# Optimization experiments

Hardware: AMD Instinct MI355X
Metric: run time of the kernel (lower is better)

Reference implementation:

```python
import jax, jax.numpy as jnp
import numpy as np

N = 4096      # (num_domains+1) * batch_size
F_IN = 512    # nfeat
HID = 64      # nhid per head
H = 8         # nheads
ALPHA = 0.2   # leaky-relu negative slope
EDGE_P = 0.01 # adjacency density


def setup_inputs() -> dict:
    key = jax.random.key(0)
    k1, k2, k3, k4 = jax.random.split(key, 4)
    x = jax.random.normal(k1, (N, F_IN), dtype=jnp.float32)
    adj = (jax.random.uniform(k2, (N, N)) < EDGE_P).astype(jnp.float32)
    # ensure self-loops so every row has at least one valid edge for softmax
    adj = jnp.maximum(adj, jnp.eye(N, dtype=jnp.float32))
    W = jax.random.normal(k3, (H, F_IN, HID), dtype=jnp.float32) * 0.1
    a = jax.random.normal(k4, (H, 2 * HID), dtype=jnp.float32) * 0.1
    return {"x": x, "adj": adj, "W": W, "a": a}


def reference(x, adj, W, a):
    # Wh: [H, N, HID] -- per-head linear projection
    Wh = jnp.einsum('nf,hfd->hnd', x, W)
    # additive attention logits: e_ij = leakyrelu(a1.Wh_i + a2.Wh_j)
    e_src = jnp.einsum('hnd,hd->hn', Wh, a[:, :HID])   # [H, N]
    e_dst = jnp.einsum('hnd,hd->hn', Wh, a[:, HID:])   # [H, N]
    e = jax.nn.leaky_relu(e_src[:, :, None] + e_dst[:, None, :], ALPHA)  # [H, N, N]
    e = jnp.where(adj[None] > 0, e, jnp.float32(-9e15))
    att = jax.nn.softmax(e, axis=-1)                    # masked softmax over neighbors
    h = jnp.einsum('hnm,hmd->hnd', att, Wh)             # [H, N, HID]
    h = jax.nn.elu(h)                                   # concat=True -> elu per head
    # concat heads: [N, H*HID]
    return jnp.transpose(h, (1, 0, 2)).reshape(N, H * HID)
```

## Files before the change

kernel.cpp:

```cpp
#include <hip/hip_runtime.h>
#include <hip/hip_bf16.h>
#include <math.h>

#define N_NODES 4096
#define F_IN    512
#define HID     64
#define H       8
#define NJ      512
#define ALPHA   0.2f

typedef __bf16 bf16x8 __attribute__((ext_vector_type(8)));
typedef float  f32x4  __attribute__((ext_vector_type(4)));

#define A_UNITS (N_NODES * F_IN / 4)
#define B_UNITS (NJ * F_IN)

__device__ __forceinline__ void split_bf16(float v, __bf16& hi, __bf16& lo) {
    hi = (__bf16)v;
    lo = (__bf16)(v - (float)hi);
}

__global__ __launch_bounds__(256) void conv_prep(const float* __restrict__ x,
                                                 const float* __restrict__ W,
                                                 __bf16* __restrict__ Ah,
                                                 __bf16* __restrict__ Al,
                                                 __bf16* __restrict__ Bth,
                                                 __bf16* __restrict__ Btl) {
    int id = blockIdx.x * 256 + threadIdx.x;
    if (id < A_UNITS) {
        float4 v = ((const float4*)x)[id];
        __bf16 h0, h1, h2, h3, l0, l1, l2, l3;
        split_bf16(v.x, h0, l0); split_bf16(v.y, h1, l1);
        split_bf16(v.z, h2, l2); split_bf16(v.w, h3, l3);
        __bf16* ph = Ah + (size_t)id * 4;
        __bf16* pl = Al + (size_t)id * 4;
        ph[0] = h0; ph[1] = h1; ph[2] = h2; ph[3] = h3;
        pl[0] = l0; pl[1] = l1; pl[2] = l2; pl[3] = l3;
    } else {
        int bid = id - A_UNITS;
        if (bid < B_UNITS) {
            int k = bid & (F_IN - 1);
            int j = bid >> 9;
            float v = W[(size_t)(j >> 6) * F_IN * HID + (size_t)k * HID + (j & 63)];
            __bf16 h, l;
            split_bf16(v, h, l);
            Bth[(size_t)j * F_IN + k] = h;
            Btl[(size_t)j * F_IN + k] = l;
        }
    }
}

__global__ __launch_bounds__(256) void wh_gemm_mfma(const __bf16* __restrict__ Ah,
                                                    const __bf16* __restrict__ Al,
                                                    const __bf16* __restrict__ Bth,
                                                    const __bf16* __restrict__ Btl,
                                                    float* __restrict__ Whf,
                                                    __bf16* __restrict__ Whb) {
    const int bm = blockIdx.x;
    const int bn = blockIdx.y;
    const int tid  = threadIdx.x;
    const int wave = tid >> 6;
    const int lane = tid & 63;
    const int lm = lane & 15;
    const int lq = lane >> 4;

    __shared__ __align__(16) __bf16 As_h[128][40];
    __shared__ __align__(16) __bf16 As_l[128][40];
    __shared__ __align__(16) __bf16 Bs_h[64][40];
    __shared__ __align__(16) __bf16 Bs_l[64][40];

    f32x4 acc[2][4];
    #pragma unroll
    for (int r = 0; r < 2; r++)
        #pragma unroll
        for (int c = 0; c < 4; c++)
            acc[r][c] = (f32x4){0.f, 0.f, 0.f, 0.f};

    for (int k0 = 0; k0 < F_IN; k0 += 32) {
        #pragma unroll
        for (int s = 0; s < 2; s++) {
            int idx = tid + s * 256;
            int m  = idx >> 2;
            int kk = (idx & 3) << 3;
            size_t g = (size_t)(bm * 128 + m) * F_IN + k0 + kk;
            *(uint4*)&As_h[m][kk] = *(const uint4*)(Ah + g);
            *(uint4*)&As_l[m][kk] = *(const uint4*)(Al + g);
        }
        {
            int n  = tid >> 2;
            int kk = (tid & 3) << 3;
            size_t g = (size_t)(bn * 64 + n) * F_IN + k0 + kk;
            *(uint4*)&Bs_h[n][kk] = *(const uint4*)(Bth + g);
            *(uint4*)&Bs_l[n][kk] = *(const uint4*)(Btl + g);
        }
        __syncthreads();

        bf16x8 afh[2], afl[2], bfh[4], bfl[4];
        #pragma unroll
        for (int r = 0; r < 2; r++) {
            int row = wave * 32 + r * 16 + lm;
            afh[r] = *(const bf16x8*)&As_h[row][lq * 8];
            afl[r] = *(const bf16x8*)&As_l[row][lq * 8];
        }
        #pragma unroll
        for (int c = 0; c < 4; c++) {
            int nrow = c * 16 + lm;
            bfh[c] = *(const bf16x8*)&Bs_h[nrow][lq * 8];
            bfl[c] = *(const bf16x8*)&Bs_l[nrow][lq * 8];
        }
        #pragma unroll
        for (int r = 0; r < 2; r++)
            #pragma unroll
            for (int c = 0; c < 4; c++) {
                acc[r][c] = __builtin_amdgcn_mfma_f32_16x16x32_bf16(afh[r], bfh[c], acc[r][c], 0, 0, 0);
                acc[r][c] = __builtin_amdgcn_mfma_f32_16x16x32_bf16(afh[r], bfl[c], acc[r][c], 0, 0, 0);
                acc[r][c] = __builtin_amdgcn_mfma_f32_16x16x32_bf16(afl[r], bfh[c], acc[r][c], 0, 0, 0);
            }
        __syncthreads();
    }

    #pragma unroll
    for (int r = 0; r < 2; r++)
        #pragma unroll
        for (int c = 0; c < 4; c++)
            #pragma unroll
            for (int reg = 0; reg < 4; reg++) {
                int row = bm * 128 + wave * 32 + r * 16 + lq * 4 + reg;
                int col = bn * 64 + c * 16 + lm;
                float v = acc[r][c][reg];
                Whf[(size_t)row * NJ + col] = v;
                Whb[(size_t)row * NJ + col] = (__bf16)v;
            }
}

__global__ __launch_bounds__(256) void src_dst(const float* __restrict__ Whf,
                                               const float* __restrict__ a,
                                               float* __restrict__ esrc,
                                               float* __restrict__ edst) {
    int gw   = blockIdx.x * 4 + (threadIdx.x >> 6);
    int lane = threadIdx.x & 63;
    int n = gw >> 3;
    int h = gw & 7;
    float v  = Whf[(size_t)n * NJ + h * HID + lane];
    float p1 = v * a[h * 2 * HID + lane];
    float p2 = v * a[h * 2 * HID + HID + lane];
    #pragma unroll
    for (int o = 32; o; o >>= 1) {
        p1 += __shfl_xor(p1, o);
        p2 += __shfl_xor(p2, o);
    }
    if (lane == 0) {
        esrc[h * N_NODES + n] = p1;
        edst[h * N_NODES + n] = p2;
    }
}

#define MAXN 192

__global__ __launch_bounds__(512) void gat_attn(const float* __restrict__ adj,
                                                const __bf16* __restrict__ Whb,
                                                const float* __restrict__ esrc,
                                                const float* __restrict__ edst,
                                                float* __restrict__ out) {
    const int i   = blockIdx.x;
    const int tid = threadIdx.x;
    __shared__ int   nbr[MAXN];
    __shared__ float att[H][MAXN];
    __shared__ float denom[H];
    __shared__ __align__(8) float2 part[256];
    __shared__ int   cnt;

    if (tid == 0) cnt = 0;
    __syncthreads();

    const float4* arow = (const float4*)(adj + (size_t)i * N_NODES);
    for (int v = tid; v < N_NODES / 4; v += 512) {
        float4 q = arow[v];
        if (q.x > 0.f) { int p = atomicAdd(&cnt, 1); if (p < MAXN) nbr[p] = v * 4 + 0; }
        if (q.y > 0.f) { int p = atomicAdd(&cnt, 1); if (p < MAXN) nbr[p] = v * 4 + 1; }
        if (q.z > 0.f) { int p = atomicAdd(&cnt, 1); if (p < MAXN) nbr[p] = v * 4 + 2; }
        if (q.w > 0.f) { int p = atomicAdd(&cnt, 1); if (p < MAXN) nbr[p] = v * 4 + 3; }
    }
    __syncthreads();
    int n = cnt;
    if (n > MAXN) n = MAXN;

    {
        const int lane = tid & 63;
        const int h    = tid >> 6;
        float es = esrc[h * N_NODES + i];
        float m = -1e30f;
        for (int j = lane; j < n; j += 64) {
            float lg = es + edst[h * N_NODES + nbr[j]];
            lg = lg > 0.f ? lg : ALPHA * lg;
            att[h][j] = lg;
            m = fmaxf(m, lg);
        }
        #pragma unroll
        for (int o = 32; o; o >>= 1) m = fmaxf(m, __shfl_xor(m, o));
        float s = 0.f;
        for (int j = lane; j < n; j += 64) {
            float w = __expf(att[h][j] - m);
            att[h][j] = w;
            s += w;
        }
        #pragma unroll
        for (int o = 32; o; o >>= 1) s += __shfl_xor(s, o);
        if (lane == 0) denom[h] = s;
    }
    __syncthreads();

    const int half = tid >> 8;
    const int t    = tid & 255;
    const int h    = t >> 5;
    const int dp   = t & 31;
    const __bf16* wb = Whb + h * HID + dp * 2;

    float acc0 = 0.f, acc1 = 0.f;
    #pragma unroll 4
    for (int j = half; j < n; j += 2) {
        int nb = nbr[j];
        float w = att[h][j];
        unsigned u = *(const unsigned*)(wb + (size_t)nb * NJ);
        float f0 = __uint_as_float(u << 16);
        float f1 = __uint_as_float(u & 0xffff0000u);
        acc0 += w * f0;
        acc1 += w * f1;
    }
    if (half == 1) part[t] = make_float2(acc0, acc1);
    __syncthreads();
    if (half == 0) {
        float2 p = part[t];
        float inv = 1.f / denom[h];
        float v0 = (acc0 + p.x) * inv;
        float v1 = (acc1 + p.y) * inv;
        v0 = v0 > 0.f ? v0 : expm1f(v0);
        v1 = v1 > 0.f ? v1 : expm1f(v1);
        *(float2*)(out + (size_t)i * NJ + h * HID + dp * 2) = make_float2(v0, v1);
    }
}

extern "C" void kernel_launch(void* const* d_in, const int* in_sizes, int n_in,
                              void* d_out, int out_size, void* d_ws, size_t ws_size,
                              hipStream_t stream) {
    const float* x   = (const float*)d_in[0];
    const float* adj = (const float*)d_in[1];
    const float* W   = (const float*)d_in[2];
    const float* a   = (const float*)d_in[3];
    float* out = (float*)d_out;

    float*  Whf  = (float*)d_ws;
    float*  esrc = Whf + (size_t)N_NODES * NJ;
    float*  edst = esrc + (size_t)H * N_NODES;
    __bf16* Whb  = (__bf16*)(edst + (size_t)H * N_NODES);
    __bf16* Ah   = Whb + (size_t)N_NODES * NJ;
    __bf16* Al   = Ah  + (size_t)N_NODES * F_IN;
    __bf16* Bth  = Al  + (size_t)N_NODES * F_IN;
    __bf16* Btl  = Bth + (size_t)NJ * F_IN;

    conv_prep<<<(A_UNITS + B_UNITS) / 256, 256, 0, stream>>>(x, W, Ah, Al, Bth, Btl);

    dim3 g1(N_NODES / 128, NJ / 64);
    wh_gemm_mfma<<<g1, 256, 0, stream>>>(Ah, Al, Bth, Btl, Whf, Whb);

    src_dst<<<(H * N_NODES) / 4, 256, 0, stream>>>(Whf, a, esrc, edst);

    gat_attn<<<N_NODES, 512, 0, stream>>>(adj, Whb, esrc, edst, out);
}
```

Before: 150.5 us.

## Fuse attention-logit reduction into GEMM epilogue and use ballot-compacted neighbor lists

Measured after the change: 158.6 us. +5.3%, slower.

```diff
diff --git a/kernel.cpp b/kernel.cpp
--- a/kernel.cpp
+++ b/kernel.cpp
@@ -50,194 +50,177 @@
     }
 }
 
-__global__ __launch_bounds__(256) void wh_gemm_mfma(const __bf16* __restrict__ Ah,
-                                                    const __bf16* __restrict__ Al,
-                                                    const __bf16* __restrict__ Bth,
-                                                    const __bf16* __restrict__ Btl,
-                                                    float* __restrict__ Whf,
-                                                    __bf16* __restrict__ Whb) {
+__global__ __launch_bounds__(256) void wh_gemm_fused(const __bf16* __restrict__ Ah,
+                                                     const __bf16* __restrict__ Al,
+                                                     const __bf16* __restrict__ Bth,
+                                                     const __bf16* __restrict__ Btl,
+                                                     const float* __restrict__ a,
+                                                     __bf16* __restrict__ Whb,
+                                                     float* __restrict__ esrc,
+                                                     float* __restrict__ edst) {
     const int bm = blockIdx.x;
-    const int bn = blockIdx.y;
+    const int h  = blockIdx.y;
     const int tid  = threadIdx.x;
     const int wave = tid >> 6;
     const int lane = tid & 63;
     const int lm = lane & 15;
     const int lq = lane >> 4;
 
-    __shared__ __align__(16) __bf16 As_h[128][40];
-    __shared__ __align__(16) __bf16 As_l[128][40];
-    __shared__ __align__(16) __bf16 Bs_h[64][40];
-    __shared__ __align__(16) __bf16 Bs_l[64][40];
-
-    f32x4 acc[2][4];
-    #pragma unroll
-    for (int r = 0; r < 2; r++)
-        #pragma unroll
-        for (int c = 0; c < 4; c++)
-            acc[r][c] = (f32x4){0.f, 0.f, 0.f, 0.f};
-
-    for (int k0 = 0; k0 < F_IN; k0 += 32) {
+    __shared__ __align__(16) __bf16 As_h[64][72];
+    __shared__ __align__(16) __bf16 As_l[64][72];
+    __shared__ __align__(16) __bf16 Bs_h[64][72];
+    __shared__ __align__(16) __bf16 Bs_l[64][72];
+
+    f32x4 acc[4];
+    #pragma unroll
+    for (int c = 0; c < 4; c++) acc[c] = (f32x4){0.f, 0.f, 0.f, 0.f};
+
+    for (int k0 = 0; k0 < F_IN; k0 += 64) {
         #pragma unroll
         for (int s = 0; s < 2; s++) {
             int idx = tid + s * 256;
-            int m  = idx >> 2;
-            int kk = (idx & 3) << 3;
-            size_t g = (size_t)(bm * 128 + m) * F_IN + k0 + kk;
-            *(uint4*)&As_h[m][kk] = *(const uint4*)(Ah + g);
-            *(uint4*)&As_l[m][kk] = *(const uint4*)(Al + g);
-        }
-        {
-            int n  = tid >> 2;
-            int kk = (tid & 3) << 3;
-            size_t g = (size_t)(bn * 64 + n) * F_IN + k0 + kk;
-            *(uint4*)&Bs_h[n][kk] = *(const uint4*)(Bth + g);
-            *(uint4*)&Bs_l[n][kk] = *(const uint4*)(Btl + g);
+            int m  = idx >> 3;
+            int kk = (idx & 7) << 3;
+            size_t ga = (size_t)(bm * 64 + m) * F_IN + k0 + kk;
+            size_t gb = (size_t)(h * 64 + m) * F_IN + k0 + kk;
+            *(uint4*)&As_h[m][kk] = *(const uint4*)(Ah + ga);
+            *(uint4*)&As_l[m][kk] = *(const uint4*)(Al + ga);
+            *(uint4*)&Bs_h[m][kk] = *(const uint4*)(Bth + gb);
+            *(uint4*)&Bs_l[m][kk] = *(const uint4*)(Btl + gb);
         }
         __syncthreads();
 
-        bf16x8 afh[2], afl[2], bfh[4], bfl[4];
-        #pragma unroll
-        for (int r = 0; r < 2; r++) {
-            int row = wave * 32 + r * 16 + lm;
-            afh[r] = *(const bf16x8*)&As_h[row][lq * 8];
-            afl[r] = *(const bf16x8*)&As_l[row][lq * 8];
-        }
-        #pragma unroll
-        for (int c = 0; c < 4; c++) {
-            int nrow = c * 16 + lm;
-            bfh[c] = *(const bf16x8*)&Bs_h[nrow][lq * 8];
-            bfl[c] = *(const bf16x8*)&Bs_l[nrow][lq * 8];
-        }
-        #pragma unroll
-        for (int r = 0; r < 2; r++)
+        #pragma unroll
+        for (int kh = 0; kh < 2; kh++) {
+            bf16x8 afh = *(const bf16x8*)&As_h[wave * 16 + lm][kh * 32 + lq * 8];
+            bf16x8 afl = *(const bf16x8*)&As_l[wave * 16 + lm][kh * 32 + lq * 8];
+            bf16x8 bh[4], bl[4];
             #pragma unroll
             for (int c = 0; c < 4; c++) {
-                acc[r][c] = __builtin_amdgcn_mfma_f32_16x16x32_bf16(afh[r], bfh[c], acc[r][c], 0, 0, 0);
-                acc[r][c] = __builtin_amdgcn_mfma_f32_16x16x32_bf16(afh[r], bfl[c], acc[r][c], 0, 0, 0);
-                acc[r][c] = __builtin_amdgcn_mfma_f32_16x16x32_bf16(afl[r], bfh[c], acc[r][c], 0, 0, 0);
+                bh[c] = *(const bf16x8*)&Bs_h[c * 16 + lm][kh * 32 + lq * 8];
+                bl[c] = *(const bf16x8*)&Bs_l[c * 16 + lm][kh * 32 + lq * 8];
             }
+            #pragma unroll
+            for (int c = 0; c < 4; c++) {
+                acc[c] = __builtin_amdgcn_mfma_f32_16x16x32_bf16(afh, bh[c], acc[c], 0, 0, 0);
+                acc[c] = __builtin_amdgcn_mfma_f32_16x16x32_bf16(afh, bl[c], acc[c], 0, 0, 0);
+                acc[c] = __builtin_amdgcn_mfma_f32_16x16x32_bf16(afl, bh[c], acc[c], 0, 0, 0);
+            }
+        }
         __syncthreads();
     }
 
-    #pragma unroll
-    for (int r = 0; r < 2; r++)
-        #pragma unroll
-        for (int c = 0; c < 4; c++)
-            #pragma unroll
-            for (int reg = 0; reg < 4; reg++) {
-                int row = bm * 128 + wave * 32 + r * 16 + lq * 4 + reg;
-                int col = bn * 64 + c * 16 + lm;
-                float v = acc[r][c][reg];
-                Whf[(size_t)row * NJ + col] = v;
-                Whb[(size_t)row * NJ + col] = (__bf16)v;
-            }
-}
-
-__global__ __launch_bounds__(256) void src_dst(const float* __restrict__ Whf,
-                                               const float* __restrict__ a,
-                                               float* __restrict__ esrc,
-                                               float* __restrict__ edst) {
-    int gw   = blockIdx.x * 4 + (threadIdx.x >> 6);
-    int lane = threadIdx.x & 63;
-    int n = gw >> 3;
-    int h = gw & 7;
-    float v  = Whf[(size_t)n * NJ + h * HID + lane];
-    float p1 = v * a[h * 2 * HID + lane];
-    float p2 = v * a[h * 2 * HID + HID + lane];
-    #pragma unroll
-    for (int o = 32; o; o >>= 1) {
-        p1 += __shfl_xor(p1, o);
-        p2 += __shfl_xor(p2, o);
-    }
-    if (lane == 0) {
-        esrc[h * N_NODES + n] = p1;
-        edst[h * N_NODES + n] = p2;
-    }
-}
-
-#define MAXN 192
+    float a1c[4], a2c[4];
+    #pragma unroll
+    for (int c = 0; c < 4; c++) {
+        a1c[c] = a[h * 2 * HID + c * 16 + lm];
+        a2c[c] = a[h * 2 * HID + HID + c * 16 + lm];
+    }
+
+    #pragma unroll
+    for (int r = 0; r < 4; r++) {
+        int row = bm * 64 + wave * 16 + lq * 4 + r;
+        float s1 = 0.f, s2 = 0.f;
+        #pragma unroll
+        for (int c = 0; c < 4; c++) {
+            float v = acc[c][r];
+            Whb[(size_t)row * NJ + h * HID + c * 16 + lm] = (__bf16)v;
+            s1 += v * a1c[c];
+            s2 += v * a2c[c];
+        }
+        #pragma unroll
+        for (int o = 1; o < 16; o <<= 1) {
+            s1 += __shfl_xor(s1, o);
+            s2 += __shfl_xor(s2, o);
+        }
+        if (lm == 0) {
+            esrc[h * N_NODES + row] = s1;
+            edst[h * N_NODES + row] = s2;
+        }
+    }
+}
+
+#define MAXN 128
 
 __global__ __launch_bounds__(512) void gat_attn(const float* __restrict__ adj,
                                                 const __bf16* __restrict__ Whb,
                                                 const float* __restrict__ esrc,
                                                 const float* __restrict__ edst,
                                                 float* __restrict__ out) {
-    const int i   = blockIdx.x;
-    const int tid = threadIdx.x;
+    const int i    = blockIdx.x;
+    const int tid  = threadIdx.x;
+    const int wave = tid >> 6;
+    const int lane = tid & 63;
     __shared__ int   nbr[MAXN];
     __shared__ float att[H][MAXN];
     __shared__ float denom[H];
-    __shared__ __align__(8) float2 part[256];
     __shared__ int   cnt;
 
     if (tid == 0) cnt = 0;
     __syncthreads();
 
+    const unsigned long long lm_lt = (1ull << lane) - 1;
     const float4* arow = (const float4*)(adj + (size_t)i * N_NODES);
-    for (int v = tid; v < N_NODES / 4; v += 512) {
-        float4 q = arow[v];
-        if (q.x > 0.f) { int p = atomicAdd(&cnt, 1); if (p < MAXN) nbr[p] = v * 4 + 0; }
-        if (q.y > 0.f) { int p = atomicAdd(&cnt, 1); if (p < MAXN) nbr[p] = v * 4 + 1; }
-        if (q.z > 0.f) { int p = atomicAdd(&cnt, 1); if (p < MAXN) nbr[p] = v * 4 + 2; }
-        if (q.w > 0.f) { int p = atomicAdd(&cnt, 1); if (p < MAXN) nbr[p] = v * 4 + 3; }
+    #pragma unroll
+    for (int c2 = 0; c2 < 2; c2++) {
+        int chunk = wave * 2 + c2;
+        float4 q = arow[chunk * 64 + lane];
+        int col0 = chunk * 256 + lane * 4;
+        float vals[4] = {q.x, q.y, q.z, q.w};
+        #pragma unroll
+        for (int k = 0; k < 4; k++) {
+            bool p = vals[k] > 0.f;
+            unsigned long long mk = __ballot(p);
+            int tot = __popcll(mk);
+            if (tot) {
+                int base = 0;
+                if (lane == 0) base = atomicAdd(&cnt, tot);
+                base = __shfl(base, 0);
+                if (p) {
+                    int pos = base + __popcll(mk & lm_lt);
+                    if (pos < MAXN) nbr[pos] = col0 + k;
+                }
+            }
+        }
     }
     __syncthreads();
     int n = cnt;
     if (n > MAXN) n = MAXN;
 
     {
-        const int lane = tid & 63;
-        const int h    = tid >> 6;
-        float es = esrc[h * N_NODES + i];
+        float es = esrc[wave * N_NODES + i];
         float m = -1e30f;
         for (int j = lane; j < n; j += 64) {
-            float lg = es + edst[h * N_NODES + nbr[j]];
+            float lg = es + edst[wave * N_NODES + nbr[j]];
             lg = lg > 0.f ? lg : ALPHA * lg;
-            att[h][j] = lg;
+            att[wave][j] = lg;
             m = fmaxf(m, lg);
         }
         #pragma unroll
         for (int o = 32; o; o >>= 1) m = fmaxf(m, __shfl_xor(m, o));
         float s = 0.f;
         for (int j = lane; j < n; j += 64) {
-            float w = __expf(att[h][j] - m);
-            att[h][j] = w;
+            float w = __expf(att[wave][j] - m);
+            att[wave][j] = w;
             s += w;
         }
         #pragma unroll
         for (int o = 32; o; o >>= 1) s += __shfl_xor(s, o);
-        if (lane == 0) denom[h] = s;
+        if (lane == 0) denom[wave] = s;
     }
     __syncthreads();
 
-    const int half = tid >> 8;
-    const int t    = tid & 255;
-    const int h    = t >> 5;
-    const int dp   = t & 31;
-    const __bf16* wb = Whb + h * HID + dp * 2;
-
-    float acc0 = 0.f, acc1 = 0.f;
+    const __bf16* wb = Whb + tid;
+    float acc0 = 0.f;
     #pragma unroll 4
-    for (int j = half; j < n; j += 2) {
+    for (int j = 0; j < n; j++) {
         int nb = nbr[j];
-        float w = att[h][j];
-        unsigned u = *(const unsigned*)(wb + (size_t)nb * NJ);
-        float f0 = __uint_as_float(u << 16);
-        float f1 = __uint_as_float(u & 0xffff0000u);
-        acc0 += w * f0;
-        acc1 += w * f1;
-    }
-    if (half == 1) part[t] = make_float2(acc0, acc1);
-    __syncthreads();
-    if (half == 0) {
-        float2 p = part[t];
-        float inv = 1.f / denom[h];
-        float v0 = (acc0 + p.x) * inv;
-        float v1 = (acc1 + p.y) * inv;
-        v0 = v0 > 0.f ? v0 : expm1f(v0);
-        v1 = v1 > 0.f ? v1 : expm1f(v1);
-        *(float2*)(out + (size_t)i * NJ + h * HID + dp * 2) = make_float2(v0, v1);
-    }
+        float w = att[wave][j];
+        unsigned short us = *(const unsigned short*)(wb + (size_t)nb * NJ);
+        acc0 += w * __uint_as_float(((unsigned)us) << 16);
+    }
+    float val = acc0 / denom[wave];
+    out[(size_t)i * NJ + tid] = val > 0.f ? val : expm1f(val);
 }
 
 extern "C" void kernel_launch(void* const* d_in, const int* in_sizes, int n_in,
@@ -249,8 +232,7 @@
     const float* a   = (const float*)d_in[3];
     float* out = (float*)d_out;
 
-    float*  Whf  = (float*)d_ws;
-    float*  esrc = Whf + (size_t)N_NODES * NJ;
+    float*  esrc = (float*)d_ws;
     float*  edst = esrc + (size_t)H * N_NODES;
     __bf16* Whb  = (__bf16*)(edst + (size_t)H * N_NODES);
     __bf16* Ah   = Whb + (size_t)N_NODES * NJ;
@@ -260,10 +242,8 @@
 
     conv_prep<<<(A_UNITS + B_UNITS) / 256, 256, 0, stream>>>(x, W, Ah, Al, Bth, Btl);
 
-    dim3 g1(N_NODES / 128, NJ / 64);
-    wh_gemm_mfma<<<g1, 256, 0, stream>>>(Ah, Al, Bth, Btl, Whf, Whb);
-
-    src_dst<<<(H * N_NODES) / 4, 256, 0, stream>>>(Whf, a, esrc, edst);
+    dim3 g1(N_NODES / 64, H);
+    wh_gemm_fused<<<g1, 256, 0, stream>>>(Ah, Al, Bth, Btl, a, Whb, esrc, edst);
 
     gat_attn<<<N_NODES, 512, 0, stream>>>(adj, Whb, esrc, edst, out);
 }
```
